# Optimization experiments

Measured on AMD Instinct MI355X. Metric: run time of the kernel, lower is better.

The kernel has to match this reference:

```python
import jax, jax.numpy as jnp
import numpy as np

B, T, D = 4, 2048, 1024
H, K, V = 4, 256, 256        # head_k_dim = head_v_dim = hidden/num_heads
M, TOPK = 256, 4             # num_slots == head_k_dim
CHUNK = 64                   # scan checkpointing granularity
SCALE = K ** -0.5            # kernel default q scale


def setup_inputs() -> dict:
    key = jax.random.key(0)
    ks = jax.random.split(key, 10)
    s = lambda i, shape, sc: jax.random.normal(ks[i], shape, jnp.float32) * sc
    return {
        "hidden_states": s(0, (B, T, D), 1.0),
        "Wq": s(1, (D, H * K), D ** -0.5),
        "Wk": s(2, (D, H * K), D ** -0.5),
        "Wv": s(3, (D, H * V), D ** -0.5),
        "Wa": s(4, (D, H), D ** -0.5),
        "Wr": s(5, (D, H * M), D ** -0.5),
        "Wb": s(6, (D, H), D ** -0.5),
        "dt": jax.random.uniform(ks[7], (H,), jnp.float32, np.log(0.001), np.log(0.1)),
        "norm_w": jnp.ones((V,), jnp.float32),
        "Wo": s(8, (H * V, D), (H * V) ** -0.5),
    }


def _l2norm(x):
    return x * jax.lax.rsqrt(jnp.sum(x * x, axis=-1, keepdims=True) + 1e-6)


def _delta_scan(q, k, v, g, beta):
    """Gated delta-rule recurrence. Time-major inputs:
    q,k,g: [T,B,H,K]; v: [T,B,H,V]; beta: [T,B,H]. Returns o: [T,B,H,V]."""
    def step(S, inp):
        qt, kt, vt, gt, bt = inp
        S = S * jnp.exp(gt)[..., None]                              # diag decay on key dim
        err = vt - jnp.einsum('bhk,bhkv->bhv', kt, S)               # delta-rule error
        S = S + kt[..., None] * (bt[..., None] * err)[..., None, :]
        o = jnp.einsum('bhk,bhkv->bhv', qt, S)
        return S, o

    @jax.checkpoint
    def chunk_fn(S, inp):
        return jax.lax.scan(step, S, inp)

    nc = T // CHUNK
    inp = tuple(x.reshape((nc, CHUNK) + x.shape[1:]) for x in (q, k, v, g, beta))
    S0 = jnp.zeros((B, H, K, V), jnp.float32)
    _, o = jax.lax.scan(chunk_fn, S0, inp)                          # o: [nc,CHUNK,B,H,V]
    return o.reshape((T,) + o.shape[2:])


def reference(hidden_states, Wq, Wk, Wv, Wa, Wr, Wb, dt, norm_w, Wo):
    h = hidden_states
    q = jax.nn.silu(h @ Wq).reshape(B, T, H, K)
    k = jax.nn.silu(h @ Wk).reshape(B, T, H, K)
    v = jax.nn.silu(h @ Wv).reshape(B, T, H, V)
    a = -jax.nn.softplus(h @ Wa) * jnp.exp(dt)                      # [B,T,H] log-decay magnitude
    rt = (h @ Wr).reshape(B, T, H, M)
    beta = jax.nn.sigmoid(h @ Wb)                                   # [B,T,H]

    # noisy top-k slot routing (eval: no noise)
    m = jax.nn.sigmoid(rt)
    w, idx = jax.lax.top_k(m, TOPK)                                 # [B,T,H,TOPK]
    mask = jnp.sum(jax.nn.one_hot(idx, M, dtype=m.dtype) * w[..., None], axis=-2)
    r = mask / (jnp.sum(mask, axis=-1, keepdims=True) + 1e-6)
    g = a[..., None] * r                                            # [B,T,H,K] (M == K)

    k = k * (1.0 - jnp.exp(g))
    q = _l2norm(q) * SCALE
    k = _l2norm(k)

    tm = lambda x: jnp.moveaxis(x, 1, 0)
    o = _delta_scan(tm(q), tm(k), tm(v), tm(g), tm(beta))           # [T,B,H,V]
    o = jnp.moveaxis(o, 0, 1)                                       # [B,T,H,V]

    # RMSNorm on head_v_dim (fp32, eps 1e-5)
    o = o * jax.lax.rsqrt(jnp.mean(o * o, axis=-1, keepdims=True) + 1e-5) * norm_w
    return o.reshape(B, T, H * V) @ Wo
```

## Files before the change

### kernel.cpp

```cpp
#include <hip/hip_runtime.h>
#include <hip/hip_bf16.h>

#define TT 2048
#define BB 4
#define HH 4
#define DD 1024

using bf16x8 = __attribute__((ext_vector_type(8))) short;
using f32x4  = __attribute__((ext_vector_type(4))) float;

__device__ __forceinline__ float wave_sum(float x) {
#pragma unroll
  for (int off = 32; off >= 1; off >>= 1) x += __shfl_xor(x, off);
  return x;
}

__device__ __forceinline__ float siluf(float x) {
  return x / (1.f + expf(-x));
}

__device__ __forceinline__ unsigned short f2bf(float f) {
  unsigned u = __float_as_uint(f);
  u = (u + 0x7fffu + ((u >> 16) & 1u)) >> 16;
  return (unsigned short)u;
}
__device__ __forceinline__ float bf2f(unsigned short b) {
  return __uint_as_float(((unsigned)b) << 16);
}
__device__ __forceinline__ unsigned pack2(float a, float b) {
  return ((unsigned)f2bf(a)) | (((unsigned)f2bf(b)) << 16);
}

__device__ __forceinline__ void gload_lds16(const void* g, void* l) {
  __builtin_amdgcn_global_load_lds(
      (const __attribute__((address_space(1))) unsigned int*)g,
      (__attribute__((address_space(3))) unsigned int*)l, 16, 0, 0);
}

#define LBAR()                                              \
  do {                                                      \
    asm volatile("s_waitcnt lgkmcnt(0)" ::: "memory");      \
    __builtin_amdgcn_s_barrier();                           \
    __builtin_amdgcn_sched_barrier(0);                      \
  } while (0)

__global__ __launch_bounds__(256) void gemm_bt(const unsigned short* __restrict__ A,
                                               const unsigned short* __restrict__ Bt,
                                               float* __restrict__ C,
                                               int M, int N, int K) {
  __shared__ unsigned short As[128 * 64];
  __shared__ unsigned short Bs[128 * 64];
  const int tid = threadIdx.x;
  const int l = tid & 63;
  const int w = tid >> 6;
  const int wm = w >> 1, wn = w & 1;
  const int bid = blockIdx.x;
  const int nt = N >> 7;
  const int swz = (bid & 7) * ((int)gridDim.x >> 3) + (bid >> 3);
  const int m0 = (swz / nt) * 128, n0 = (swz % nt) * 128;

  f32x4 acc[4][4];
#pragma unroll
  for (int i = 0; i < 4; ++i)
#pragma unroll
    for (int j = 0; j < 4; ++j) acc[i][j] = (f32x4){0.f, 0.f, 0.f, 0.f};

  size_t asrc[4], bsrc[4];
  int ldst[4];
#pragma unroll
  for (int it = 0; it < 4; ++it) {
    int chunk = (it * 4 + w) * 64 + l;
    int row = chunk >> 3, s = chunk & 7;
    size_t soff = (size_t)row * K + ((s ^ (row & 7)) << 3);
    asrc[it] = (size_t)m0 * K + soff;
    bsrc[it] = (size_t)n0 * K + soff;
    ldst[it] = chunk * 8;
  }
  int ra_off[2][4], rb_off[2][4];
#pragma unroll
  for (int kh = 0; kh < 2; ++kh)
#pragma unroll
    for (int f = 0; f < 4; ++f) {
      int rowA = wm * 64 + f * 16 + (l & 15);
      ra_off[kh][f] = rowA * 128 + (((kh * 4 + (l >> 4)) ^ (rowA & 7)) << 4);
      int rowB = wn * 64 + f * 16 + (l & 15);
      rb_off[kh][f] = rowB * 128 + (((kh * 4 + (l >> 4)) ^ (rowB & 7)) << 4);
    }

  for (int k0 = 0; k0 < K; k0 += 64) {
    __syncthreads();
#pragma unroll
    for (int it = 0; it < 4; ++it) {
      gload_lds16(A + asrc[it] + k0, As + ldst[it] - l * 8);
      gload_lds16(Bt + bsrc[it] + k0, Bs + ldst[it] - l * 8);
    }
    __syncthreads();
#pragma unroll
    for (int kh = 0; kh < 2; ++kh) {
      bf16x8 af[4], bfv[4];
#pragma unroll
      for (int f = 0; f < 4; ++f) {
        af[f] = *(const bf16x8*)((const char*)As + ra_off[kh][f]);
        bfv[f] = *(const bf16x8*)((const char*)Bs + rb_off[kh][f]);
      }
#pragma unroll
      for (int i = 0; i < 4; ++i)
#pragma unroll
        for (int j = 0; j < 4; ++j)
          acc[i][j] = __builtin_amdgcn_mfma_f32_16x16x32_bf16(af[i], bfv[j],
                                                              acc[i][j], 0, 0, 0);
    }
  }
  const int cn = n0 + wn * 64 + (l & 15);
  const int rbase = m0 + wm * 64 + ((l >> 4) << 2);
#pragma unroll
  for (int i = 0; i < 4; ++i)
#pragma unroll
    for (int j = 0; j < 4; ++j)
#pragma unroll
      for (int r = 0; r < 4; ++r)
        C[(size_t)(rbase + i * 16 + r) * N + cn + j * 16] = acc[i][j][r];
}

__global__ __launch_bounds__(256) void gemm_bt3(const unsigned short* __restrict__ Ah,
                                                const unsigned short* __restrict__ Al,
                                                const unsigned short* __restrict__ Bh,
                                                const unsigned short* __restrict__ Bl,
                                                float* __restrict__ C,
                                                int M, int N, int K) {
  __shared__ unsigned short Ash[128 * 64];
  __shared__ unsigned short Asl[128 * 64];
  __shared__ unsigned short Bsh[128 * 64];
  __shared__ unsigned short Bsl[128 * 64];
  const int tid = threadIdx.x;
  const int l = tid & 63;
  const int w = tid >> 6;
  const int wm = w >> 1, wn = w & 1;
  const int bid = blockIdx.x;
  const int nt = N >> 7;
  const int swz = (bid & 7) * ((int)gridDim.x >> 3) + (bid >> 3);
  const int m0 = (swz / nt) * 128, n0 = (swz % nt) * 128;

  f32x4 acc[4][4];
#pragma unroll
  for (int i = 0; i < 4; ++i)
#pragma unroll
    for (int j = 0; j < 4; ++j) acc[i][j] = (f32x4){0.f, 0.f, 0.f, 0.f};

  size_t asrc[4], bsrc[4];
  int ldst[4];
#pragma unroll
  for (int it = 0; it < 4; ++it) {
    int chunk = (it * 4 + w) * 64 + l;
    int row = chunk >> 3, s = chunk & 7;
    size_t soff = (size_t)row * K + ((s ^ (row & 7)) << 3);
    asrc[it] = (size_t)m0 * K + soff;
    bsrc[it] = (size_t)n0 * K + soff;
    ldst[it] = chunk * 8;
  }
  int ra_off[2][4], rb_off[2][4];
#pragma unroll
  for (int kh = 0; kh < 2; ++kh)
#pragma unroll
    for (int f = 0; f < 4; ++f) {
      int rowA = wm * 64 + f * 16 + (l & 15);
      ra_off[kh][f] = rowA * 128 + (((kh * 4 + (l >> 4)) ^ (rowA & 7)) << 4);
      int rowB = wn * 64 + f * 16 + (l & 15);
      rb_off[kh][f] = rowB * 128 + (((kh * 4 + (l >> 4)) ^ (rowB & 7)) << 4);
    }

  for (int k0 = 0; k0 < K; k0 += 64) {
    __syncthreads();
#pragma unroll
    for (int it = 0; it < 4; ++it) {
      gload_lds16(Ah + asrc[it] + k0, Ash + ldst[it] - l * 8);
      gload_lds16(Al + asrc[it] + k0, Asl + ldst[it] - l * 8);
      gload_lds16(Bh + bsrc[it] + k0, Bsh + ldst[it] - l * 8);
      gload_lds16(Bl + bsrc[it] + k0, Bsl + ldst[it] - l * 8);
    }
    __syncthreads();
#pragma unroll
    for (int kh = 0; kh < 2; ++kh) {
      bf16x8 afh[4], bfh[4], tmp[4];
#pragma unroll
      for (int f = 0; f < 4; ++f) {
        afh[f] = *(const bf16x8*)((const char*)Ash + ra_off[kh][f]);
        bfh[f] = *(const bf16x8*)((const char*)Bsh + rb_off[kh][f]);
      }
#pragma unroll
      for (int i = 0; i < 4; ++i)
#pragma unroll
        for (int j = 0; j < 4; ++j)
          acc[i][j] = __builtin_amdgcn_mfma_f32_16x16x32_bf16(afh[i], bfh[j],
                                                              acc[i][j], 0, 0, 0);
#pragma unroll
      for (int f = 0; f < 4; ++f)
        tmp[f] = *(const bf16x8*)((const char*)Asl + ra_off[kh][f]);
#pragma unroll
      for (int i = 0; i < 4; ++i)
#pragma unroll
        for (int j = 0; j < 4; ++j)
          acc[i][j] = __builtin_amdgcn_mfma_f32_16x16x32_bf16(tmp[i], bfh[j],
                                                              acc[i][j], 0, 0, 0);
#pragma unroll
      for (int f = 0; f < 4; ++f)
        tmp[f] = *(const bf16x8*)((const char*)Bsl + rb_off[kh][f]);
#pragma unroll
      for (int i = 0; i < 4; ++i)
#pragma unroll
        for (int j = 0; j < 4; ++j)
          acc[i][j] = __builtin_amdgcn_mfma_f32_16x16x32_bf16(afh[i], tmp[j],
                                                              acc[i][j], 0, 0, 0);
    }
  }
  const int cn = n0 + wn * 64 + (l & 15);
  const int rbase = m0 + wm * 64 + ((l >> 4) << 2);
#pragma unroll
  for (int i = 0; i < 4; ++i)
#pragma unroll
    for (int j = 0; j < 4; ++j)
#pragma unroll
      for (int r = 0; r < 4; ++r)
        C[(size_t)(rbase + i * 16 + r) * N + cn + j * 16] = acc[i][j][r];
}

__global__ __launch_bounds__(256) void cast2_bf16_kernel(const float* __restrict__ in,
                                                         unsigned short* __restrict__ hi,
                                                         unsigned short* __restrict__ lo) {
  const size_t i = ((size_t)blockIdx.x * 256 + threadIdx.x) * 4;
  float4 x = *(const float4*)(in + i);
  ushort4 h4, l4;
  h4.x = f2bf(x.x); l4.x = f2bf(x.x - bf2f(h4.x));
  h4.y = f2bf(x.y); l4.y = f2bf(x.y - bf2f(h4.y));
  h4.z = f2bf(x.z); l4.z = f2bf(x.z - bf2f(h4.z));
  h4.w = f2bf(x.w); l4.w = f2bf(x.w - bf2f(h4.w));
  *(ushort4*)(hi + i) = h4;
  *(ushort4*)(lo + i) = l4;
}

__global__ __launch_bounds__(256) void tcast_all_kernel(
    const float* __restrict__ Wq, const float* __restrict__ Wk,
    const float* __restrict__ Wv, const float* __restrict__ Wo,
    const float* __restrict__ Wr, unsigned short* __restrict__ WT0,
    unsigned short* __restrict__ WTrH, unsigned short* __restrict__ WTrL) {
  __shared__ float tile[32][33];
  const int which = blockIdx.x >> 10;
  const int bid = blockIdx.x & 1023;
  const int bx = bid & 31, by = bid >> 5;
  const float* W = (which == 0) ? Wq
                   : (which == 1) ? Wk
                   : (which == 2) ? Wv
                   : (which == 3) ? Wo
                                  : Wr;
  const int tx = threadIdx.x, ty = threadIdx.y;
  const int c0 = bx * 32, r0 = by * 32;
#pragma unroll
  for (int i = 0; i < 4; ++i)
    tile[ty + 8 * i][tx] = W[(size_t)(r0 + ty + 8 * i) * 1024 + c0 + tx];
  __syncthreads();
  if (which < 4) {
    unsigned short* WT = WT0 + (size_t)which * 1048576;
#pragma unroll
    for (int i = 0; i < 4; ++i)
      WT[(size_t)(c0 + ty + 8 * i) * 1024 + r0 + tx] = f2bf(tile[tx][ty + 8 * i]);
  } else {
#pragma unroll
    for (int i = 0; i < 4; ++i) {
      float x = tile[tx][ty + 8 * i];
      unsigned short h = f2bf(x);
      WTrH[(size_t)(c0 + ty + 8 * i) * 1024 + r0 + tx] = h;
      WTrL[(size_t)(c0 + ty + 8 * i) * 1024 + r0 + tx] = f2bf(x - bf2f(h));
    }
  }
}

__global__ __launch_bounds__(256) void routing_kernel(
    const float* __restrict__ hidden, const float* __restrict__ Wa,
    const float* __restrict__ Wb, const float* __restrict__ dt,
    const float* __restrict__ rproj, float* __restrict__ qkv,
    float* __restrict__ gbuf, float* __restrict__ betaT) {
  const int row = blockIdx.x;
  const int b = row >> 11;
  const int t = row & (TT - 1);
  const int h = threadIdx.x >> 6;
  const int l = threadIdx.x & 63;
  const size_t base_q = (size_t)row * 3072 + h * 256;
  const size_t base_k = base_q + 1024;
  const size_t base_r = (size_t)row * DD + h * 256;

  const float* hrow = hidden + (size_t)row * DD;
  float aa = 0.f, bb = 0.f;
#pragma unroll
  for (int i = 0; i < 16; ++i) {
    float hv = hrow[l + 64 * i];
    aa = fmaf(hv, Wa[(l + 64 * i) * HH + h], aa);
    bb = fmaf(hv, Wb[(l + 64 * i) * HH + h], bb);
  }
  aa = wave_sum(aa);
  bb = wave_sum(bb);
  float sp = (aa > 20.f) ? aa : log1pf(expf(aa));
  float a_ = -sp * expf(dt[h]);
  float beta = 1.f / (1.f + expf(-bb));
  const int bh = b * HH + h;
  if (l == 0) betaT[(size_t)bh * TT + t] = beta;

  float4 rt4 = *(const float4*)(rproj + base_r + l * 4);
  float rv[4] = {rt4.x, rt4.y, rt4.z, rt4.w};
  int used = 0;
  int widx[4];
  float wsig[4], wg[4], wkfac[4];
#pragma unroll
  for (int it = 0; it < 4; ++it) {
    float bv = -3.4e38f;
    int bi = 0x7fffffff;
#pragma unroll
    for (int c = 0; c < 4; ++c) {
      bool ok = !(used & (1 << c));
      float v = rv[c];
      if (ok && (v > bv)) {
        bv = v;
        bi = l * 4 + c;
      }
    }
#pragma unroll
    for (int off = 32; off >= 1; off >>= 1) {
      float ov = __shfl_xor(bv, off);
      int oi = __shfl_xor(bi, off);
      if (ov > bv || (ov == bv && oi < bi)) {
        bv = ov;
        bi = oi;
      }
    }
    widx[it] = bi;
    wsig[it] = 1.f / (1.f + expf(-bv));
    if ((bi >> 2) == l) used |= 1 << (bi & 3);
  }
  float wsum = wsig[0] + wsig[1] + wsig[2] + wsig[3] + 1e-6f;
#pragma unroll
  for (int it = 0; it < 4; ++it) {
    float g = a_ * (wsig[it] / wsum);
    wg[it] = g;
    wkfac[it] = 1.f - expf(g);
  }

  float4 kv4 = *(const float4*)(qkv + base_k + l * 4);
  float kvv[4] = {kv4.x, kv4.y, kv4.z, kv4.w};
  float kmask[4], ddv[4];
#pragma unroll
  for (int c = 0; c < 4; ++c) {
    int slot = l * 4 + c;
    float f = 0.f, d = 0.f;
#pragma unroll
    for (int it = 0; it < 4; ++it) {
      bool hit = (slot == widx[it]);
      f = hit ? wkfac[it] : f;
      d = hit ? wg[it] : d;
    }
    kmask[c] = siluf(kvv[c]) * f;
    ddv[c] = d;
  }
  float ss = kmask[0] * kmask[0] + kmask[1] * kmask[1] + kmask[2] * kmask[2] +
             kmask[3] * kmask[3];
  ss = wave_sum(ss);
  float kn = rsqrtf(ss + 1e-6f);
  *(float4*)(qkv + base_k + l * 4) =
      make_float4(kmask[0] * kn, kmask[1] * kn, kmask[2] * kn, kmask[3] * kn);
  *(float4*)(gbuf + ((size_t)bh * TT + t) * 256 + l * 4) =
      make_float4(ddv[0], ddv[1], ddv[2], ddv[3]);

  float4 qv4 = *(const float4*)(qkv + base_q + l * 4);
  float qs[4] = {siluf(qv4.x), siluf(qv4.y), siluf(qv4.z), siluf(qv4.w)};
  float qss = qs[0] * qs[0] + qs[1] * qs[1] + qs[2] * qs[2] + qs[3] * qs[3];
  qss = wave_sum(qss);
  float qn = rsqrtf(qss + 1e-6f) * 0.0625f;
  *(float4*)(qkv + base_q + l * 4) =
      make_float4(qs[0] * qn, qs[1] * qn, qs[2] * qn, qs[3] * qn);
}

__global__ __launch_bounds__(256) void phaseA_kernel(
    const float* __restrict__ qkv,
    float* __restrict__ expcG,
    const float* __restrict__ betaT, unsigned short* __restrict__ TinvB,
    unsigned short* __restrict__ AB, unsigned short* __restrict__ Wg,
    unsigned short* __restrict__ Qg, unsigned short* __restrict__ XTg) {
  __shared__ unsigned short XB[64 * 256];
  __shared__ unsigned short QW[128 * 256];
  __shared__ float Mb[64 * 68];
  const int bid = blockIdx.x;
  const int bh = bid >> 5, c = bid & 31;
  const int b = bh >> 2, h = bh & 3;
  const int t0 = c * 64;
  const int tid = threadIdx.x;
  const int w = tid >> 6, l = tid & 63;
  const int ln = l & 15, lg = l >> 4;

  {
    float cacc = 0.f;
    const int slot = tid >> 3, byt = tid & 7;
#pragma unroll 4
    for (int i = 0; i < 64; ++i) {
      size_t ga = ((size_t)bh * TT + t0 + i) * 256 + tid;
      size_t pq = (size_t)(b * TT + t0 + i) * 3072 + h * 256 + tid;
      cacc += expcG[ga];
      float e = expf(cacc);
      float ei = __builtin_amdgcn_rcpf(e);
      float qv = qkv[pq];
      float kv = qkv[pq + 1024];
      unsigned short wb = f2bf(kv * e);
      unsigned short qb = f2bf(qv * e);
      unsigned short xb = f2bf(kv * ei);
      Wg[ga] = wb;
      Qg[ga] = qb;
      int sw = ((slot ^ (i & 7)) << 3) + byt;
      XB[i * 256 + sw] = xb;
      QW[i * 256 + sw] = qb;
      QW[(i + 64) * 256 + sw] = wb;
      if (i == 63) expcG[ga] = e;
    }
  }
  __syncthreads();

  f32x4 acc[2][4];
#pragma unroll
  for (int tr = 0; tr < 2; ++tr)
#pragma unroll
    for (int tc = 0; tc < 4; ++tc) acc[tr][tc] = (f32x4){0.f, 0.f, 0.f, 0.f};
  const int R0 = w * 32;
#pragma unroll
  for (int kt = 0; kt < 8; ++kt) {
    const int ks = kt * 4 + lg;
    const int ra0 = R0 + ln, ra1 = R0 + 16 + ln;
    bf16x8 a0 = *(const bf16x8*)&QW[ra0 * 256 + ((ks ^ (ra0 & 7)) << 3)];
    bf16x8 a1 = *(const bf16x8*)&QW[ra1 * 256 + ((ks ^ (ra1 & 7)) << 3)];
#pragma unroll
    for (int tc = 0; tc < 4; ++tc) {
      const int br = tc * 16 + ln;
      bf16x8 bf_ = *(const bf16x8*)&XB[br * 256 + ((ks ^ (br & 7)) << 3)];
      acc[0][tc] = __builtin_amdgcn_mfma_f32_16x16x32_bf16(a0, bf_, acc[0][tc], 0, 0, 0);
      acc[1][tc] = __builtin_amdgcn_mfma_f32_16x16x32_bf16(a1, bf_, acc[1][tc], 0, 0, 0);
    }
  }
  const size_t gb = (((size_t)bh * 32 + c) << 12);
  if (w < 2) {
#pragma unroll
    for (int tr = 0; tr < 2; ++tr)
#pragma unroll
      for (int tc = 0; tc < 4; ++tc)
#pragma unroll
        for (int r = 0; r < 4; ++r) {
          int i = R0 + tr * 16 + lg * 4 + r;
          int s = tc * 16 + ln;
          AB[gb + i * 64 + s] = (s <= i) ? f2bf(acc[tr][tc][r]) : (unsigned short)0;
        }
  } else {
#pragma unroll
    for (int tr = 0; tr < 2; ++tr)
#pragma unroll
      for (int tc = 0; tc < 4; ++tc)
#pragma unroll
        for (int r = 0; r < 4; ++r) {
          int i = R0 - 64 + tr * 16 + lg * 4 + r;
          Mb[i * 68 + tc * 16 + ln] = acc[tr][tc][r];
        }
  }
  __syncthreads();

  if (w == 0) {
    float tcol[64];
#pragma unroll
    for (int i = 0; i < 64; ++i) {
      float bi = betaT[(size_t)bh * TT + t0 + i];
      float a_ = (l == i) ? 1.f : 0.f;
#pragma unroll
      for (int s = 0; s < i; ++s)
        a_ = fmaf(-bi * Mb[i * 68 + s], tcol[s], a_);
      tcol[i] = a_;
    }
#pragma unroll
    for (int s = 0; s < 64; ++s) Mb[s * 68 + l] = tcol[s];
  } else {
    const int kk1 = tid - 64;
#pragma unroll 1
    for (int pass = 0; pass < 2; ++pass) {
      if (pass == 1 && kk1 >= 64) break;
      const int k = (pass == 0) ? kk1 : (192 + kk1);
      unsigned short* dst = XTg + ((size_t)bh * 256 + k) * TT + t0;
      const int kslot = k >> 3, kb = k & 7;
#pragma unroll 1
      for (int jq = 0; jq < 8; ++jq) {
        unsigned short e[8];
#pragma unroll
        for (int j = 0; j < 8; ++j) {
          int t = jq * 8 + j;
          e[j] = XB[t * 256 + (((kslot ^ (t & 7)) << 3) + kb)];
        }
        uint4 o;
        o.x = ((unsigned)e[0]) | (((unsigned)e[1]) << 16);
        o.y = ((unsigned)e[2]) | (((unsigned)e[3]) << 16);
        o.z = ((unsigned)e[4]) | (((unsigned)e[5]) << 16);
        o.w = ((unsigned)e[6]) | (((unsigned)e[7]) << 16);
        *(uint4*)(dst + jq * 8) = o;
      }
    }
  }
  __syncthreads();
  {
    const int i = tid >> 2;
    const int sb = (tid & 3) * 16;
#pragma unroll
    for (int mq = 0; mq < 4; ++mq) {
      float v0 = Mb[i * 68 + sb + mq * 4 + 0];
      float v1 = Mb[i * 68 + sb + mq * 4 + 1];
      float v2 = Mb[i * 68 + sb + mq * 4 + 2];
      float v3 = Mb[i * 68 + sb + mq * 4 + 3];
      uint2 p;
      p.x = pack2(v0, v1);
      p.y = pack2(v2, v3);
      *(uint2*)(TinvB + gb + (size_t)i * 64 + sb + mq * 4) = p;
    }
  }
}

__global__ __launch_bounds__(256) void chunk_scan_kernel(
    const unsigned short* __restrict__ Wg, const unsigned short* __restrict__ Qg,
    const unsigned short* __restrict__ XTg, const unsigned short* __restrict__ Tb,
    const unsigned short* __restrict__ Ab, const float* __restrict__ qkv,
    const float* __restrict__ expcG, const float* __restrict__ betaT,
    float* __restrict__ obuf) {
  __shared__ unsigned short ShL[16 * 256];
  __shared__ unsigned short SlL[16 * 256];
  __shared__ unsigned short R2bL[16 * 64];
  __shared__ unsigned short UbL[16 * 64];
  const int bid = blockIdx.x;
  const int bh = bid & 15, slice = bid >> 4;
  const int b = bh >> 2, h = bh & 3;
  const int tid = threadIdx.x;
  const int w = tid >> 6;
  const int l = tid & 63;
  const int ln = l & 15, lg = l >> 4;

  const unsigned short* Wbh = Wg + (size_t)bh * TT * 256;
  const unsigned short* Qbh = Qg + (size_t)bh * TT * 256;
  const unsigned short* XTbh = XTg + (size_t)bh * 256 * TT;
  const unsigned short* Tbh = Tb + (size_t)bh * 32 * 4096;
  const unsigned short* Abh = Ab + (size_t)bh * 32 * 4096;
  const float* betabh = betaT + (size_t)bh * TT;
  const float* ebh = expcG + (size_t)bh * TT * 256;

  f32x4 S0 = {0.f, 0.f, 0.f, 0.f}, S1 = S0, S2 = S0, S3 = S0;

  const int ru_off =
      ln * 64 + ((((w * 2) + (lg >> 1)) ^ (ln & 7)) << 3) + (lg & 1) * 4;

  bf16x8 wA[8], qA[8], wB[8], qB[8];
  float4 vA, bA, vB, bB;

#define LOADWQV(W_, Q_, V_, B_, c_)                                            \
  {                                                                            \
    const int t0_ = (c_) * 64;                                                 \
    _Pragma("unroll") for (int kt = 0; kt < 8; ++kt) {                         \
      const size_t arow =                                                      \
          (size_t)(t0_ + w * 16 + ln) * 256 + kt * 32 + lg * 8;                \
      W_[kt] = *(const bf16x8*)(Wbh + arow);                                   \
      Q_[kt] = *(const bf16x8*)(Qbh + arow);                                   \
    }                                                                          \
    const size_t vrow = (size_t)(b * TT + t0_ + w * 16 + lg * 4) * 3072 +      \
                        2048 + h * 256 + slice * 16 + ln;                      \
    V_.x = siluf(qkv[vrow]);                                                   \
    V_.y = siluf(qkv[vrow + 3072]);                                            \
    V_.z = siluf(qkv[vrow + 2 * 3072]);                                        \
    V_.w = siluf(qkv[vrow + 3 * 3072]);                                        \
    B_ = *(const float4*)(betabh + t0_ + w * 16 + lg * 4);                     \
  }

#define SSTORE(S_, E_, mt_)                                                    \
  {                                                                            \
    S_[0] *= E_.x;                                                             \
    S_[1] *= E_.y;                                                             \
    S_[2] *= E_.z;                                                             \
    S_[3] *= E_.w;                                                             \
    ushort4 hp, lp;                                                            \
    hp.x = f2bf(S_[0]); lp.x = f2bf(S_[0] - bf2f(hp.x));                       \
    hp.y = f2bf(S_[1]); lp.y = f2bf(S_[1] - bf2f(hp.y));                       \
    hp.z = f2bf(S_[2]); lp.z = f2bf(S_[2] - bf2f(hp.z));                       \
    hp.w = f2bf(S_[3]); lp.w = f2bf(S_[3] - bf2f(hp.w));                       \
    const int so_ = ln * 256 +                                                 \
                    ((((w * 8) + (mt_)*2 + (lg >> 1)) ^ ln) << 3) +            \
                    (lg & 1) * 4;                                              \
    *(ushort4*)(&ShL[so_]) = hp;                                               \
    *(ushort4*)(&SlL[so_]) = lp;                                               \
  }

#define CHUNK(Wc, Qc, Vc, Bc, Wn, Qn, Vn, Bn, c_)                              \
  {                                                                            \
    const int c = (c_);                                                        \
    const size_t tb_base = (size_t)c * 4096 + (w * 16 + ln) * 64 + lg * 8;     \
    bf16x8 tf0 = *(const bf16x8*)(Tbh + tb_base);                              \
    bf16x8 tf1 = *(const bf16x8*)(Tbh + tb_base + 32);                         \
    bf16x8 af0 = *(const bf16x8*)(Abh + tb_base);                              \
    bf16x8 af1 = *(const bf16x8*)(Abh + tb_base + 32);                         \
    const size_t xb = (size_t)(w * 64 + ln) * TT + c * 64 + lg * 8;            \
    bf16x8 xf0a = *(const bf16x8*)(XTbh + xb);                                 \
    bf16x8 xf0b = *(const bf16x8*)(XTbh + xb + 32);                            \
    bf16x8 xf1a = *(const bf16x8*)(XTbh + xb + 16 * TT);                       \
    bf16x8 xf1b = *(const bf16x8*)(XTbh + xb + 16 * TT + 32);                  \
    bf16x8 xf2a = *(const bf16x8*)(XTbh + xb + 32 * TT);                       \
    bf16x8 xf2b = *(const bf16x8*)(XTbh + xb + 32 * TT + 32);                  \
    bf16x8 xf3a = *(const bf16x8*)(XTbh + xb + 48 * TT);                       \
    bf16x8 xf3b = *(const bf16x8*)(XTbh + xb + 48 * TT + 32);                  \
    const float* ebase = ebh + (size_t)(c * 64 + 63) * 256 + w * 64 + lg * 4;  \
    float4 eL0 = *(const float4*)(ebase);                                      \
    float4 eL1 = *(const float4*)(ebase + 16);                                 \
    float4 eL2 = *(const float4*)(ebase + 32);                                 \
    float4 eL3 = *(const float4*)(ebase + 48);                                 \
    f32x4 rhs = {0.f, 0.f, 0.f, 0.f}, oq = {0.f, 0.f, 0.f, 0.f};               \
    if (c > 0) {                                                               \
      _Pragma("unroll") for (int kt = 0; kt < 8; ++kt) {                       \
        const int sro = ln * 256 + (((kt * 4 + lg) ^ ln) << 3);                \
        bf16x8 sh = *(const bf16x8*)(&ShL[sro]);                               \
        bf16x8 sl = *(const bf16x8*)(&SlL[sro]);                               \
        rhs = __builtin_amdgcn_mfma_f32_16x16x32_bf16(Wc[kt], sh, rhs, 0, 0, 0); \
        rhs = __builtin_amdgcn_mfma_f32_16x16x32_bf16(Wc[kt], sl, rhs, 0, 0, 0); \
        oq = __builtin_amdgcn_mfma_f32_16x16x32_bf16(Qc[kt], sh, oq, 0, 0, 0); \
        oq = __builtin_amdgcn_mfma_f32_16x16x32_bf16(Qc[kt], sl, oq, 0, 0, 0); \
      }                                                                        \
    }                                                                          \
    if (c + 1 < 32) LOADWQV(Wn, Qn, Vn, Bn, c + 1);                            \
    {                                                                          \
      ushort4 r2p;                                                             \
      r2p.x = f2bf(Bc.x * (Vc.x - rhs[0]));                                    \
      r2p.y = f2bf(Bc.y * (Vc.y - rhs[1]));                                    \
      r2p.z = f2bf(Bc.z * (Vc.z - rhs[2]));                                    \
      r2p.w = f2bf(Bc.w * (Vc.w - rhs[3]));                                    \
      *(ushort4*)(&R2bL[ru_off]) = r2p;                                        \
    }                                                                          \
    LBAR();                                                                    \
    {                                                                          \
      bf16x8 rf0 = *(const bf16x8*)(&R2bL[ln * 64 + (((0 + lg) ^ (ln & 7)) << 3)]); \
      bf16x8 rf1 = *(const bf16x8*)(&R2bL[ln * 64 + (((4 + lg) ^ (ln & 7)) << 3)]); \
      f32x4 u = {0.f, 0.f, 0.f, 0.f};                                          \
      u = __builtin_amdgcn_mfma_f32_16x16x32_bf16(tf0, rf0, u, 0, 0, 0);       \
      u = __builtin_amdgcn_mfma_f32_16x16x32_bf16(tf1, rf1, u, 0, 0, 0);       \
      ushort4 up;                                                              \
      up.x = f2bf(u[0]);                                                       \
      up.y = f2bf(u[1]);                                                       \
      up.z = f2bf(u[2]);                                                       \
      up.w = f2bf(u[3]);                                                       \
      *(ushort4*)(&UbL[ru_off]) = up;                                          \
    }                                                                          \
    LBAR();                                                                    \
    bf16x8 uf0 = *(const bf16x8*)(&UbL[ln * 64 + (((0 + lg) ^ (ln & 7)) << 3)]); \
    bf16x8 uf1 = *(const bf16x8*)(&UbL[ln * 64 + (((4 + lg) ^ (ln & 7)) << 3)]); \
    {                                                                          \
      f32x4 o = oq;                                                            \
      o = __builtin_amdgcn_mfma_f32_16x16x32_bf16(af0, uf0, o, 0, 0, 0);       \
      o = __builtin_amdgcn_mfma_f32_16x16x32_bf16(af1, uf1, o, 0, 0, 0);       \
      const size_t orow =                                                      \
          ((size_t)(b * TT + c * 64 + w * 16 + lg * 4) * HH + h) * 256 +       \
          slice * 16 + ln;                                                     \
      obuf[orow] = o[0];                                                       \
      obuf[orow + HH * 256] = o[1];                                            \
      obuf[orow + 2 * HH * 256] = o[2];                                        \
      obuf[orow + 3 * HH * 256] = o[3];                                        \
    }                                                                          \
    S0 = __builtin_amdgcn_mfma_f32_16x16x32_bf16(xf0a, uf0, S0, 0, 0, 0);      \
    S0 = __builtin_amdgcn_mfma_f32_16x16x32_bf16(xf0b, uf1, S0, 0, 0, 0);      \
    S1 = __builtin_amdgcn_mfma_f32_16x16x32_bf16(xf1a, uf0, S1, 0, 0, 0);      \
    S1 = __builtin_amdgcn_mfma_f32_16x16x32_bf16(xf1b, uf1, S1, 0, 0, 0);      \
    S2 = __builtin_amdgcn_mfma_f32_16x16x32_bf16(xf2a, uf0, S2, 0, 0, 0);      \
    S2 = __builtin_amdgcn_mfma_f32_16x16x32_bf16(xf2b, uf1, S2, 0, 0, 0);      \
    S3 = __builtin_amdgcn_mfma_f32_16x16x32_bf16(xf3a, uf0, S3, 0, 0, 0);      \
    S3 = __builtin_amdgcn_mfma_f32_16x16x32_bf16(xf3b, uf1, S3, 0, 0, 0);      \
    SSTORE(S0, eL0, 0);                                                        \
    SSTORE(S1, eL1, 1);                                                        \
    SSTORE(S2, eL2, 2);                                                        \
    SSTORE(S3, eL3, 3);                                                        \
    LBAR();                                                                    \
  }

  LOADWQV(wA, qA, vA, bA, 0);
  for (int cc = 0; cc < 32; cc += 2) {
    CHUNK(wA, qA, vA, bA, wB, qB, vB, bB, cc);
    CHUNK(wB, qB, vB, bB, wA, qA, vA, bA, cc + 1);
  }
#undef CHUNK
#undef SSTORE
#undef LOADWQV
}

__global__ __launch_bounds__(256) void rmsnorm_bf16_kernel(
    const float* __restrict__ o, const float* __restrict__ w,
    unsigned short* __restrict__ out) {
  const int row = blockIdx.x;
  const int l = threadIdx.x & 63;
  const size_t base = (size_t)row * DD + (threadIdx.x >> 6) * 256 + l * 4;
  float4 x = *(const float4*)(o + base);
  float ss = x.x * x.x + x.y * x.y + x.z * x.z + x.w * x.w;
  ss = wave_sum(ss);
  float sc = rsqrtf(ss * (1.f / 256.f) + 1e-5f);
  float4 wv = *(const float4*)(w + l * 4);
  ushort4 o4;
  o4.x = f2bf(x.x * sc * wv.x);
  o4.y = f2bf(x.y * sc * wv.y);
  o4.z = f2bf(x.z * sc * wv.z);
  o4.w = f2bf(x.w * sc * wv.w);
  *(ushort4*)(out + base) = o4;
}

extern "C" void kernel_launch(void* const* d_in, const int* in_sizes, int n_in,
                              void* d_out, int out_size, void* d_ws,
                              size_t ws_size, hipStream_t stream) {
  const float* hidden = (const float*)d_in[0];
  const float* Wq = (const float*)d_in[1];
  const float* Wk = (const float*)d_in[2];
  const float* Wv = (const float*)d_in[3];
  const float* Wa = (const float*)d_in[4];
  const float* Wr = (const float*)d_in[5];
  const float* Wb = (const float*)d_in[6];
  const float* dt = (const float*)d_in[7];
  const float* norm_w = (const float*)d_in[8];
  const float* Wo = (const float*)d_in[9];
  float* out = (float*)d_out;

  const size_t NP = (size_t)BB * TT * DD;
  float* ws = (float*)d_ws;
  float* qkv = ws;
  float* gbuf = ws + 3 * NP;
  unsigned short* hbf = (unsigned short*)(ws + 4 * NP);
  unsigned short* wT = (unsigned short*)(ws + 4 * NP + NP / 2);
  unsigned short* WT0 = wT;
  unsigned short* WT3 = wT + 3 * 1048576;
  unsigned short* WT4 = wT + 4 * 1048576;
  unsigned short* WT5 = wT + 5 * 1048576;
  float* betaT = ws + 4 * NP + NP / 2 + 3 * 1024 * 1024;
  float* after_beta = betaT + 16 * TT;
  unsigned short* Qg = (unsigned short*)after_beta;
  unsigned short* XTg = Qg + NP;
  unsigned short* Ab = XTg + NP;
  unsigned short* Wgb = hbf;
  unsigned short* Tbb = WT4;
  unsigned short* hlo = (unsigned short*)qkv;
  float* rproj = out;

  dim3 bt(256);
  cast2_bf16_kernel<<<8192, 256, 0, stream>>>(hidden, hbf, hlo);
  tcast_all_kernel<<<5120, dim3(32, 8), 0, stream>>>(Wq, Wk, Wv, Wo, Wr, WT0,
                                                     WT4, WT5);

  gemm_bt3<<<512, bt, 0, stream>>>(hbf, hlo, WT4, WT5, rproj, 8192, 1024, 1024);
  gemm_bt<<<1536, bt, 0, stream>>>(hbf, WT0, qkv, 8192, 3072, 1024);

  routing_kernel<<<8192, 256, 0, stream>>>(hidden, Wa, Wb, dt, rproj, qkv,
                                           gbuf, betaT);
  phaseA_kernel<<<512, 256, 0, stream>>>(qkv, gbuf, betaT, Tbb, Ab, Wgb, Qg,
                                         XTg);
  chunk_scan_kernel<<<256, 256, 0, stream>>>(Wgb, Qg, XTg, Tbb, Ab, qkv, gbuf,
                                             betaT, out);
  rmsnorm_bf16_kernel<<<8192, 256, 0, stream>>>(out, norm_w, hbf);
  gemm_bt<<<512, bt, 0, stream>>>(hbf, WT3, out, 8192, 1024, 1024);
}
```

Before: 435.7 us.

## Fuse routing top-k and q/k normalization into phaseA chunk kernel

Removes the separate per-row routing kernel. phaseA now computes, per 64-step chunk, the a/beta projections, the top-k slot selection and the q/k L2 norm factors, keeping them in shared memory. It then applies silu, the routing mask and the norms on the fly while building the cumulative decays. This avoids writing normalized q/k back to qkv and materializing the full g buffer, which removes a large round trip through global memory and one launch. The cost is serial routing work inside only 512 blocks, which lowers parallelism for that phase.

```diff
diff --git a/kernel.cpp b/kernel.cpp
--- a/kernel.cpp
+++ b/kernel.cpp
@@ -274,118 +274,19 @@
   }
 }
 
-__global__ __launch_bounds__(256) void routing_kernel(
+__global__ __launch_bounds__(256) void phaseA_kernel(
     const float* __restrict__ hidden, const float* __restrict__ Wa,
     const float* __restrict__ Wb, const float* __restrict__ dt,
-    const float* __restrict__ rproj, float* __restrict__ qkv,
-    float* __restrict__ gbuf, float* __restrict__ betaT) {
-  const int row = blockIdx.x;
-  const int b = row >> 11;
-  const int t = row & (TT - 1);
-  const int h = threadIdx.x >> 6;
-  const int l = threadIdx.x & 63;
-  const size_t base_q = (size_t)row * 3072 + h * 256;
-  const size_t base_k = base_q + 1024;
-  const size_t base_r = (size_t)row * DD + h * 256;
-
-  const float* hrow = hidden + (size_t)row * DD;
-  float aa = 0.f, bb = 0.f;
-#pragma unroll
-  for (int i = 0; i < 16; ++i) {
-    float hv = hrow[l + 64 * i];
-    aa = fmaf(hv, Wa[(l + 64 * i) * HH + h], aa);
-    bb = fmaf(hv, Wb[(l + 64 * i) * HH + h], bb);
-  }
-  aa = wave_sum(aa);
-  bb = wave_sum(bb);
-  float sp = (aa > 20.f) ? aa : log1pf(expf(aa));
-  float a_ = -sp * expf(dt[h]);
-  float beta = 1.f / (1.f + expf(-bb));
-  const int bh = b * HH + h;
-  if (l == 0) betaT[(size_t)bh * TT + t] = beta;
-
-  float4 rt4 = *(const float4*)(rproj + base_r + l * 4);
-  float rv[4] = {rt4.x, rt4.y, rt4.z, rt4.w};
-  int used = 0;
-  int widx[4];
-  float wsig[4], wg[4], wkfac[4];
-#pragma unroll
-  for (int it = 0; it < 4; ++it) {
-    float bv = -3.4e38f;
-    int bi = 0x7fffffff;
-#pragma unroll
-    for (int c = 0; c < 4; ++c) {
-      bool ok = !(used & (1 << c));
-      float v = rv[c];
-      if (ok && (v > bv)) {
-        bv = v;
-        bi = l * 4 + c;
-      }
-    }
-#pragma unroll
-    for (int off = 32; off >= 1; off >>= 1) {
-      float ov = __shfl_xor(bv, off);
-      int oi = __shfl_xor(bi, off);
-      if (ov > bv || (ov == bv && oi < bi)) {
-        bv = ov;
-        bi = oi;
-      }
-    }
-    widx[it] = bi;
-    wsig[it] = 1.f / (1.f + expf(-bv));
-    if ((bi >> 2) == l) used |= 1 << (bi & 3);
-  }
-  float wsum = wsig[0] + wsig[1] + wsig[2] + wsig[3] + 1e-6f;
-#pragma unroll
-  for (int it = 0; it < 4; ++it) {
-    float g = a_ * (wsig[it] / wsum);
-    wg[it] = g;
-    wkfac[it] = 1.f - expf(g);
-  }
-
-  float4 kv4 = *(const float4*)(qkv + base_k + l * 4);
-  float kvv[4] = {kv4.x, kv4.y, kv4.z, kv4.w};
-  float kmask[4], ddv[4];
-#pragma unroll
-  for (int c = 0; c < 4; ++c) {
-    int slot = l * 4 + c;
-    float f = 0.f, d = 0.f;
-#pragma unroll
-    for (int it = 0; it < 4; ++it) {
-      bool hit = (slot == widx[it]);
-      f = hit ? wkfac[it] : f;
-      d = hit ? wg[it] : d;
-    }
-    kmask[c] = siluf(kvv[c]) * f;
-    ddv[c] = d;
-  }
-  float ss = kmask[0] * kmask[0] + kmask[1] * kmask[1] + kmask[2] * kmask[2] +
-             kmask[3] * kmask[3];
-  ss = wave_sum(ss);
-  float kn = rsqrtf(ss + 1e-6f);
-  *(float4*)(qkv + base_k + l * 4) =
-      make_float4(kmask[0] * kn, kmask[1] * kn, kmask[2] * kn, kmask[3] * kn);
-  *(float4*)(gbuf + ((size_t)bh * TT + t) * 256 + l * 4) =
-      make_float4(ddv[0], ddv[1], ddv[2], ddv[3]);
-
-  float4 qv4 = *(const float4*)(qkv + base_q + l * 4);
-  float qs[4] = {siluf(qv4.x), siluf(qv4.y), siluf(qv4.z), siluf(qv4.w)};
-  float qss = qs[0] * qs[0] + qs[1] * qs[1] + qs[2] * qs[2] + qs[3] * qs[3];
-  qss = wave_sum(qss);
-  float qn = rsqrtf(qss + 1e-6f) * 0.0625f;
-  *(float4*)(qkv + base_q + l * 4) =
-      make_float4(qs[0] * qn, qs[1] * qn, qs[2] * qn, qs[3] * qn);
-}
-
-__global__ __launch_bounds__(256) void phaseA_kernel(
-    const float* __restrict__ qkv,
-    float* __restrict__ expcG,
-    const float* __restrict__ betaT, unsigned short* __restrict__ TinvB,
-    unsigned short* __restrict__ AB, unsigned short* __restrict__ Wg,
-    unsigned short* __restrict__ Qg, unsigned short* __restrict__ XTg) {
+    const float* __restrict__ rproj, const float* __restrict__ qkv,
+    float* __restrict__ expcG, float* __restrict__ betaT,
+    unsigned short* __restrict__ TinvB, unsigned short* __restrict__ AB,
+    unsigned short* __restrict__ Wg, unsigned short* __restrict__ Qg,
+    unsigned short* __restrict__ XTg) {
   __shared__ unsigned short XB[64 * 256];
   __shared__ unsigned short QW[128 * 256];
   __shared__ float Mb[64 * 68];
+  __shared__ int widxL[64][4];
+  __shared__ float wgL[64][4], wkfacL[64][4], knL[64], qnL[64], betaL[64];
   const int bid = blockIdx.x;
   const int bh = bid >> 5, c = bid & 31;
   const int b = bh >> 2, h = bh & 3;
@@ -395,17 +296,127 @@
   const int ln = l & 15, lg = l >> 4;
 
   {
+    const float edt = expf(dt[h]);
+    float waR[16], wbR[16];
+#pragma unroll
+    for (int i = 0; i < 16; ++i) {
+      waR[i] = Wa[(l + 64 * i) * HH + h];
+      wbR[i] = Wb[(l + 64 * i) * HH + h];
+    }
+#pragma unroll 1
+    for (int j = 0; j < 16; ++j) {
+      const int r = w * 16 + j;
+      const size_t grow = (size_t)(b * TT + t0 + r);
+      const float* hrow = hidden + grow * DD;
+      float aa = 0.f, bb = 0.f;
+#pragma unroll
+      for (int i = 0; i < 16; ++i) {
+        float hv = hrow[l + 64 * i];
+        aa = fmaf(hv, waR[i], aa);
+        bb = fmaf(hv, wbR[i], bb);
+      }
+      aa = wave_sum(aa);
+      bb = wave_sum(bb);
+      float sp = (aa > 20.f) ? aa : log1pf(expf(aa));
+      float a_ = -sp * edt;
+      float beta = 1.f / (1.f + expf(-bb));
+
+      float4 rt4 = *(const float4*)(rproj + grow * DD + h * 256 + l * 4);
+      float rv[4] = {rt4.x, rt4.y, rt4.z, rt4.w};
+      int used = 0;
+      int widx[4];
+      float wsig[4], wg_[4], wkfac_[4];
+#pragma unroll
+      for (int it = 0; it < 4; ++it) {
+        float bv = -3.4e38f;
+        int bi = 0x7fffffff;
+#pragma unroll
+        for (int cc = 0; cc < 4; ++cc) {
+          bool ok = !(used & (1 << cc));
+          float v = rv[cc];
+          if (ok && (v > bv)) {
+            bv = v;
+            bi = l * 4 + cc;
+          }
+        }
+#pragma unroll
+        for (int off = 32; off >= 1; off >>= 1) {
+          float ov = __shfl_xor(bv, off);
+          int oi = __shfl_xor(bi, off);
+          if (ov > bv || (ov == bv && oi < bi)) {
+            bv = ov;
+            bi = oi;
+          }
+        }
+        widx[it] = bi;
+        wsig[it] = 1.f / (1.f + expf(-bv));
+        if ((bi >> 2) == l) used |= 1 << (bi & 3);
+      }
+      float wsum = wsig[0] + wsig[1] + wsig[2] + wsig[3] + 1e-6f;
+#pragma unroll
+      for (int it = 0; it < 4; ++it) {
+        float g = a_ * (wsig[it] / wsum);
+        wg_[it] = g;
+        wkfac_[it] = 1.f - expf(g);
+      }
+
+      float4 kv4 = *(const float4*)(qkv + grow * 3072 + 1024 + h * 256 + l * 4);
+      float kvv[4] = {kv4.x, kv4.y, kv4.z, kv4.w};
+      float ssum = 0.f;
+#pragma unroll
+      for (int cc = 0; cc < 4; ++cc) {
+        int slot = l * 4 + cc;
+        float f = 0.f;
+#pragma unroll
+        for (int it = 0; it < 4; ++it)
+          f = (slot == widx[it]) ? wkfac_[it] : f;
+        float km = siluf(kvv[cc]) * f;
+        ssum += km * km;
+      }
+      ssum = wave_sum(ssum);
+      float kn = rsqrtf(ssum + 1e-6f);
+
+      float4 qv4 = *(const float4*)(qkv + grow * 3072 + h * 256 + l * 4);
+      float qs0 = siluf(qv4.x), qs1 = siluf(qv4.y), qs2 = siluf(qv4.z),
+            qs3 = siluf(qv4.w);
+      float qss = qs0 * qs0 + qs1 * qs1 + qs2 * qs2 + qs3 * qs3;
+      qss = wave_sum(qss);
+      float qn = rsqrtf(qss + 1e-6f) * 0.0625f;
+
+      if (l == 0) {
+        betaL[r] = beta;
+        knL[r] = kn;
+        qnL[r] = qn;
+#pragma unroll
+        for (int it = 0; it < 4; ++it) {
+          widxL[r][it] = widx[it];
+          wgL[r][it] = wg_[it];
+          wkfacL[r][it] = wkfac_[it];
+        }
+        betaT[(size_t)bh * TT + t0 + r] = beta;
+      }
+    }
+  }
+  __syncthreads();
+
+  {
     float cacc = 0.f;
     const int slot = tid >> 3, byt = tid & 7;
 #pragma unroll 4
     for (int i = 0; i < 64; ++i) {
       size_t ga = ((size_t)bh * TT + t0 + i) * 256 + tid;
       size_t pq = (size_t)(b * TT + t0 + i) * 3072 + h * 256 + tid;
-      cacc += expcG[ga];
+      int w0 = widxL[i][0], w1 = widxL[i][1], w2 = widxL[i][2], w3 = widxL[i][3];
+      float g = 0.f, f = 0.f;
+      if (tid == w0) { g = wgL[i][0]; f = wkfacL[i][0]; }
+      if (tid == w1) { g = wgL[i][1]; f = wkfacL[i][1]; }
+      if (tid == w2) { g = wgL[i][2]; f = wkfacL[i][2]; }
+      if (tid == w3) { g = wgL[i][3]; f = wkfacL[i][3]; }
+      cacc += g;
       float e = expf(cacc);
       float ei = __builtin_amdgcn_rcpf(e);
-      float qv = qkv[pq];
-      float kv = qkv[pq + 1024];
+      float qv = siluf(qkv[pq]) * qnL[i];
+      float kv = siluf(qkv[pq + 1024]) * f * knL[i];
       unsigned short wb = f2bf(kv * e);
       unsigned short qb = f2bf(qv * e);
       unsigned short xb = f2bf(kv * ei);
@@ -469,7 +480,7 @@
     float tcol[64];
 #pragma unroll
     for (int i = 0; i < 64; ++i) {
-      float bi = betaT[(size_t)bh * TT + t0 + i];
+      float bi = betaL[i];
       float a_ = (l == i) ? 1.f : 0.f;
 #pragma unroll
       for (int s = 0; s < i; ++s)
@@ -750,10 +761,8 @@
   gemm_bt3<<<512, bt, 0, stream>>>(hbf, hlo, WT4, WT5, rproj, 8192, 1024, 1024);
   gemm_bt<<<1536, bt, 0, stream>>>(hbf, WT0, qkv, 8192, 3072, 1024);
 
-  routing_kernel<<<8192, 256, 0, stream>>>(hidden, Wa, Wb, dt, rproj, qkv,
-                                           gbuf, betaT);
-  phaseA_kernel<<<512, 256, 0, stream>>>(qkv, gbuf, betaT, Tbb, Ab, Wgb, Qg,
-                                         XTg);
+  phaseA_kernel<<<512, 256, 0, stream>>>(hidden, Wa, Wb, dt, rproj, qkv, gbuf,
+                                         betaT, Tbb, Ab, Wgb, Qg, XTg);
   chunk_scan_kernel<<<256, 256, 0, stream>>>(Wgb, Qg, XTg, Tbb, Ab, qkv, gbuf,
                                              betaT, out);
   rmsnorm_bf16_kernel<<<8192, 256, 0, stream>>>(out, norm_w, hbf);
```

Measured after the change: 548.4 us. 1.26x slower.
